# Kernel tuning notes

Hardware: AMD Instinct MI355X
Metric: run time of the kernel (lower is better)

The kernel has to match this reference:

```python
import jax, jax.numpy as jnp
import numpy as np

N_NODES = 100000
N_EDGES = 1600000
D_IN = 128
D_OUT = 128


def setup_inputs() -> dict:
    key = jax.random.key(0)
    k1, k2, k3 = jax.random.split(key, 3)
    x = jax.random.normal(k1, (N_NODES, D_IN), dtype=jnp.float32)
    edge_index = jax.random.randint(k2, (2, N_EDGES), 0, N_NODES, dtype=jnp.int64)
    # Xavier-uniform-like init for weight (matches nn.init.xavier_uniform_ scale)
    limit = float(np.sqrt(6.0 / (D_IN + D_OUT)))
    weight = jax.random.uniform(k3, (D_IN, D_OUT), dtype=jnp.float32,
                                minval=-limit, maxval=limit)
    bias = jnp.zeros((D_OUT,), dtype=jnp.float32)
    return {"x": x, "edge_index": edge_index, "weight": weight, "bias": bias}


def reference(x, edge_index, weight, bias):
    num_nodes = x.shape[0]
    src = edge_index[0]  # edge_index_i: gather side
    dst = edge_index[1]  # edge_index_j: scatter side

    # Degree of each node counted over src endpoints.
    deg = jax.ops.segment_sum(jnp.ones_like(src, dtype=x.dtype), src,
                              num_segments=num_nodes)
    # deg^{-1/2} with inf -> 0 for isolated nodes.
    deg_safe = jnp.where(deg > 0, deg, jnp.ones_like(deg))
    deg_inv_sqrt = jnp.where(deg > 0, jax.lax.rsqrt(deg_safe), jnp.zeros_like(deg))

    norm = deg_inv_sqrt[src] * deg_inv_sqrt[dst]  # [E]

    h = x @ weight  # [N, D_OUT]
    # Edge-parallel gather, scale, scatter-add.
    msgs = norm[:, None] * h[src]  # [E, D_OUT]
    out = jax.ops.segment_sum(msgs, dst, num_segments=num_nodes)  # [N, D_OUT]
    return out + bias
```

## Files before the change

### kernel.cpp

```cpp
#include <hip/hip_runtime.h>

#define D 128
#define CAP 64
#define STRIP_LOG 15
#define STRIP (1 << STRIP_LOG)
#define WORDS_LOG (STRIP_LOG - 2)
#define WORDS (1 << WORDS_LOG)
#define NCHUNK 128
#define LDK 132

typedef __attribute__((ext_vector_type(8))) short bf16x8;
typedef __attribute__((ext_vector_type(4))) float f32x4;

__device__ __forceinline__ unsigned f2bf(float f) {
    unsigned u = __float_as_uint(f);
    return (u + 0x7fffu + ((u >> 16) & 1u)) >> 16;
}

__device__ __forceinline__ int chunk_size(int n_edges) {
    return (((n_edges + NCHUNK - 1) / NCHUNK) + 3) & ~3;
}

__global__ __launch_bounds__(256) void k_histA(const int* __restrict__ src,
                                               const int* __restrict__ dst,
                                               unsigned* __restrict__ pb_s,
                                               unsigned* __restrict__ pb_d, int n_edges) {
    int strip = blockIdx.x / NCHUNK, chunk = blockIdx.x % NCHUNK;
    int lo = strip << STRIP_LOG;
    __shared__ unsigned hs[WORDS];
    __shared__ unsigned hd[WORDS];
    for (int i = threadIdx.x; i < WORDS; i += 256) { hs[i] = 0; hd[i] = 0; }
    __syncthreads();

    int csz = chunk_size(n_edges);
    int beg = chunk * csz;
    int end = min(beg + csz, n_edges);
    if (beg < end) {
        int aend = beg + ((end - beg) & ~3);
        for (int i = beg + threadIdx.x * 4; i + 3 < aend; i += 1024) {
            int4 s = *(const int4*)(src + i);
            int4 d = *(const int4*)(dst + i);
            unsigned b;
            b = (unsigned)(s.x - lo); if (b < STRIP) atomicAdd(&hs[b >> 2], 1u << ((b & 3) * 8));
            b = (unsigned)(s.y - lo); if (b < STRIP) atomicAdd(&hs[b >> 2], 1u << ((b & 3) * 8));
            b = (unsigned)(s.z - lo); if (b < STRIP) atomicAdd(&hs[b >> 2], 1u << ((b & 3) * 8));
            b = (unsigned)(s.w - lo); if (b < STRIP) atomicAdd(&hs[b >> 2], 1u << ((b & 3) * 8));
            b = (unsigned)(d.x - lo); if (b < STRIP) atomicAdd(&hd[b >> 2], 1u << ((b & 3) * 8));
            b = (unsigned)(d.y - lo); if (b < STRIP) atomicAdd(&hd[b >> 2], 1u << ((b & 3) * 8));
            b = (unsigned)(d.z - lo); if (b < STRIP) atomicAdd(&hd[b >> 2], 1u << ((b & 3) * 8));
            b = (unsigned)(d.w - lo); if (b < STRIP) atomicAdd(&hd[b >> 2], 1u << ((b & 3) * 8));
        }
        for (int e = aend + threadIdx.x; e < end; e += 256) {
            unsigned bs = (unsigned)(src[e] - lo);
            if (bs < STRIP) atomicAdd(&hs[bs >> 2], 1u << ((bs & 3) * 8));
            unsigned bd = (unsigned)(dst[e] - lo);
            if (bd < STRIP) atomicAdd(&hd[bd >> 2], 1u << ((bd & 3) * 8));
        }
    }
    __syncthreads();
    unsigned* ps = pb_s + (size_t)blockIdx.x * WORDS;
    unsigned* pd = pb_d + (size_t)blockIdx.x * WORDS;
    for (int i = threadIdx.x; i < WORDS; i += 256) { ps[i] = hs[i]; pd[i] = hd[i]; }
}

__global__ __launch_bounds__(256) void k_base_dis(unsigned* __restrict__ pb_d,
                                                  const unsigned* __restrict__ pb_s,
                                                  int* __restrict__ deg_dst,
                                                  float* __restrict__ dis,
                                                  int n, int nwords) {
    int gw = blockIdx.x * 256 + threadIdx.x;
    if (gw >= nwords) return;
    int strip = gw >> WORDS_LOG, widx = gw & (WORDS - 1);
    size_t base = (size_t)strip * NCHUNK * WORDS + widx;

    unsigned run[4] = {0, 0, 0, 0};
    for (int c = 0; c < NCHUNK; ++c) {
        size_t idx = base + (size_t)c * WORDS;
        unsigned v = pb_d[idx];
        pb_d[idx] = run[0] | (run[1] << 8) | (run[2] << 16) | (run[3] << 24);
        run[0] += v & 0xffu;
        run[1] += (v >> 8) & 0xffu;
        run[2] += (v >> 16) & 0xffu;
        run[3] += (v >> 24) & 0xffu;
    }
    int g0 = (strip << STRIP_LOG) + widx * 4;
    if (g0 >= n) return;

    unsigned ss[4] = {0, 0, 0, 0};
    for (int c = 0; c < NCHUNK; ++c) {
        unsigned v = pb_s[base + (size_t)c * WORDS];
        ss[0] += v & 0xffu;
        ss[1] += (v >> 8) & 0xffu;
        ss[2] += (v >> 16) & 0xffu;
        ss[3] += (v >> 24) & 0xffu;
    }
    if (g0 + 3 < n) {
        *(int4*)(deg_dst + g0) = make_int4(run[0], run[1], run[2], run[3]);
        *(float4*)(dis + g0) = make_float4(
            ss[0] ? rsqrtf((float)ss[0]) : 0.0f, ss[1] ? rsqrtf((float)ss[1]) : 0.0f,
            ss[2] ? rsqrtf((float)ss[2]) : 0.0f, ss[3] ? rsqrtf((float)ss[3]) : 0.0f);
    } else {
        #pragma unroll
        for (int j = 0; j < 4; ++j)
            if (g0 + j < n) {
                deg_dst[g0 + j] = run[j];
                dis[g0 + j] = ss[j] ? rsqrtf((float)ss[j]) : 0.0f;
            }
    }
}

__global__ __launch_bounds__(256) void k_placeB(const int* __restrict__ src,
                                                const int* __restrict__ dst,
                                                const unsigned* __restrict__ pb_d,
                                                int* __restrict__ epad, int n_edges) {
    int strip = blockIdx.x / NCHUNK, chunk = blockIdx.x % NCHUNK;
    int lo = strip << STRIP_LOG;
    __shared__ unsigned cur[WORDS];
    const unsigned* cb = pb_d + (size_t)blockIdx.x * WORDS;
    for (int i = threadIdx.x; i < WORDS; i += 256) cur[i] = cb[i];
    __syncthreads();

    int csz = chunk_size(n_edges);
    int beg = chunk * csz;
    int end = min(beg + csz, n_edges);
    if (beg < end) {
        int aend = beg + ((end - beg) & ~3);
        for (int i = beg + threadIdx.x * 4; i + 3 < aend; i += 1024) {
            int4 s = *(const int4*)(src + i);
            int4 d = *(const int4*)(dst + i);
            unsigned b, o, r;
            b = (unsigned)(d.x - lo);
            if (b < STRIP) {
                o = atomicAdd(&cur[b >> 2], 1u << ((b & 3) * 8));
                r = (o >> ((b & 3) * 8)) & 0xffu;
                if (r < CAP) epad[(((unsigned)lo + b) << 6) + r] = s.x;
            }
            b = (unsigned)(d.y - lo);
            if (b < STRIP) {
                o = atomicAdd(&cur[b >> 2], 1u << ((b & 3) * 8));
                r = (o >> ((b & 3) * 8)) & 0xffu;
                if (r < CAP) epad[(((unsigned)lo + b) << 6) + r] = s.y;
            }
            b = (unsigned)(d.z - lo);
            if (b < STRIP) {
                o = atomicAdd(&cur[b >> 2], 1u << ((b & 3) * 8));
                r = (o >> ((b & 3) * 8)) & 0xffu;
                if (r < CAP) epad[(((unsigned)lo + b) << 6) + r] = s.z;
            }
            b = (unsigned)(d.w - lo);
            if (b < STRIP) {
                o = atomicAdd(&cur[b >> 2], 1u << ((b & 3) * 8));
                r = (o >> ((b & 3) * 8)) & 0xffu;
                if (r < CAP) epad[(((unsigned)lo + b) << 6) + r] = s.w;
            }
        }
        for (int e = aend + threadIdx.x; e < end; e += 256) {
            unsigned b = (unsigned)(dst[e] - lo);
            if (b < STRIP) {
                unsigned o = atomicAdd(&cur[b >> 2], 1u << ((b & 3) * 8));
                unsigned r = (o >> ((b & 3) * 8)) & 0xffu;
                if (r < CAP) epad[(((unsigned)lo + b) << 6) + r] = src[e];
            }
        }
    }
}

__global__ __launch_bounds__(256) void k_gemm(const float* __restrict__ x,
                                              const float* __restrict__ w,
                                              const float* __restrict__ dis,
                                              unsigned* __restrict__ hb, int nrows) {
    __shared__ __align__(16) unsigned short smem[2][128][LDK];
    int tid = threadIdx.x;
    int row0 = blockIdx.x * 128;
    int nr = min(128, nrows - row0);

    {
        const float4* w4 = (const float4*)w;
        for (int i = tid; i < 128 * 32; i += 256) {
            int k = i >> 5, n0 = (i & 31) * 4;
            float4 v = w4[i];
            smem[1][n0 + 0][k] = (unsigned short)f2bf(v.x);
            smem[1][n0 + 1][k] = (unsigned short)f2bf(v.y);
            smem[1][n0 + 2][k] = (unsigned short)f2bf(v.z);
            smem[1][n0 + 3][k] = (unsigned short)f2bf(v.w);
        }
    }
    {
        const float4* x4 = (const float4*)(x + (size_t)row0 * D);
        for (int i = tid; i < 128 * 32; i += 256) {
            int r = i >> 5, c4 = (i & 31) * 4;
            float4 v = (r < nr) ? x4[i] : make_float4(0.f, 0.f, 0.f, 0.f);
            unsigned lo = f2bf(v.x) | (f2bf(v.y) << 16);
            unsigned hi = f2bf(v.z) | (f2bf(v.w) << 16);
            *(uint2*)&smem[0][r][c4] = make_uint2(lo, hi);
        }
    }
    __syncthreads();

    int lane = tid & 63, wv = tid >> 6;
    int m = lane & 15, quad = lane >> 4;
    int rbase = wv * 32;

    f32x4 acc[2][8] = {};
    #pragma unroll
    for (int kt = 0; kt < 4; ++kt) {
        int k0 = kt * 32 + quad * 8;
        bf16x8 a0 = *(const bf16x8*)&smem[0][rbase + m][k0];
        bf16x8 a1 = *(const bf16x8*)&smem[0][rbase + 16 + m][k0];
        bf16x8 b[8];
        #pragma unroll
        for (int ct = 0; ct < 8; ++ct)
            b[ct] = *(const bf16x8*)&smem[1][ct * 16 + m][k0];
        #pragma unroll
        for (int ct = 0; ct < 8; ++ct) {
            acc[0][ct] = __builtin_amdgcn_mfma_f32_16x16x32_bf16(a0, b[ct], acc[0][ct], 0, 0, 0);
            acc[1][ct] = __builtin_amdgcn_mfma_f32_16x16x32_bf16(a1, b[ct], acc[1][ct], 0, 0, 0);
        }
    }

    __syncthreads();
    float* sO = (float*)smem;
    #pragma unroll
    for (int rt = 0; rt < 2; ++rt)
        #pragma unroll
        for (int ct = 0; ct < 8; ++ct)
            #pragma unroll
            for (int reg = 0; reg < 4; ++reg)
                sO[(rbase + rt * 16 + quad * 4 + reg) * LDK + ct * 16 + m] = acc[rt][ct][reg];
    __syncthreads();

    int r = tid >> 1, hf = tid & 1;
    if (r < nr) {
        float dn = dis[row0 + r];
        const float* so = sO + r * LDK + hf * 64;
        unsigned* hrow = hb + (size_t)(row0 + r) * 64 + hf * 32;
        #pragma unroll
        for (int j = 0; j < 8; ++j) {
            float2 p0 = *(const float2*)(so + j * 8 + 0);
            float2 p1 = *(const float2*)(so + j * 8 + 2);
            float2 p2 = *(const float2*)(so + j * 8 + 4);
            float2 p3 = *(const float2*)(so + j * 8 + 6);
            uint4 o;
            o.x = f2bf(dn * p0.x) | (f2bf(dn * p0.y) << 16);
            o.y = f2bf(dn * p1.x) | (f2bf(dn * p1.y) << 16);
            o.z = f2bf(dn * p2.x) | (f2bf(dn * p2.y) << 16);
            o.w = f2bf(dn * p3.x) | (f2bf(dn * p3.y) << 16);
            *(uint4*)(hrow + j * 4) = o;
        }
    }
}

#define ACC8(u) do { \
    ax[0] += __uint_as_float((u).x << 16); ax[1] += __uint_as_float((u).x & 0xffff0000u); \
    ax[2] += __uint_as_float((u).y << 16); ax[3] += __uint_as_float((u).y & 0xffff0000u); \
    ax[4] += __uint_as_float((u).z << 16); ax[5] += __uint_as_float((u).z & 0xffff0000u); \
    ax[6] += __uint_as_float((u).w << 16); ax[7] += __uint_as_float((u).w & 0xffff0000u); } while (0)

__global__ __launch_bounds__(256) void k_accum(const int* __restrict__ epad,
                                               const int* __restrict__ degd,
                                               const uint4* __restrict__ hb4,
                                               const float* __restrict__ dis,
                                               const float* __restrict__ bias,
                                               float* __restrict__ out, int n) {
    int wid = threadIdx.x >> 6, lane = threadIdx.x & 63;
    int node = blockIdx.x * 4 + wid;
    if (node >= n) return;
    int deg = min(degd[node], CAP);
    int g = lane >> 4, c = lane & 15;
    const int* ep = epad + (size_t)node * CAP;

    float ax[8] = {0.f, 0.f, 0.f, 0.f, 0.f, 0.f, 0.f, 0.f};
    int e = g;
    for (; e + 12 < deg; e += 16) {
        int s0 = ep[e];
        int s1 = ep[e + 4];
        int s2 = ep[e + 8];
        int s3 = ep[e + 12];
        uint4 u0 = hb4[(size_t)s0 * 16 + c];
        uint4 u1 = hb4[(size_t)s1 * 16 + c];
        uint4 u2 = hb4[(size_t)s2 * 16 + c];
        uint4 u3 = hb4[(size_t)s3 * 16 + c];
        ACC8(u0); ACC8(u1); ACC8(u2); ACC8(u3);
    }
    for (; e < deg; e += 4) {
        int s0 = ep[e];
        uint4 u0 = hb4[(size_t)s0 * 16 + c];
        ACC8(u0);
    }

    #pragma unroll
    for (int k = 0; k < 8; ++k) {
        ax[k] += __shfl_xor(ax[k], 16, 64);
        ax[k] += __shfl_xor(ax[k], 32, 64);
    }

    if (g == 0) {
        float dn = dis[node];
        float4 b0 = ((const float4*)bias)[c * 2];
        float4 b1 = ((const float4*)bias)[c * 2 + 1];
        float4 o0 = make_float4(fmaf(dn, ax[0], b0.x), fmaf(dn, ax[1], b0.y),
                                fmaf(dn, ax[2], b0.z), fmaf(dn, ax[3], b0.w));
        float4 o1 = make_float4(fmaf(dn, ax[4], b1.x), fmaf(dn, ax[5], b1.y),
                                fmaf(dn, ax[6], b1.z), fmaf(dn, ax[7], b1.w));
        float4* op = (float4*)(out + (size_t)node * D) + c * 2;
        op[0] = o0;
        op[1] = o1;
    }
}

extern "C" void kernel_launch(void* const* d_in, const int* in_sizes, int n_in,
                              void* d_out, int out_size, void* d_ws, size_t ws_size,
                              hipStream_t stream) {
    const float* x    = (const float*)d_in[0];
    const int*   ei   = (const int*)d_in[1];
    const float* w    = (const float*)d_in[2];
    const float* bias = (const float*)d_in[3];
    float* out = (float*)d_out;

    int n_edges = in_sizes[1] / 2;
    int n_nodes = in_sizes[0] / D;
    const int* src = ei;
    const int* dst = ei + n_edges;

    int nstrips = (n_nodes + STRIP - 1) >> STRIP_LOG;
    int nwords = nstrips * WORDS;

    char* ws = (char*)d_ws;
    unsigned* hb = (unsigned*)ws;      ws += (size_t)n_nodes * 64 * sizeof(unsigned);
    int* epad    = (int*)ws;           ws += (size_t)n_nodes * CAP * sizeof(int);
    int* deg_dst = (int*)ws;           ws += (size_t)n_nodes * sizeof(int);
    float* dis   = (float*)ws;         ws += (size_t)n_nodes * sizeof(float);
    unsigned* pb_s = (unsigned*)ws;    ws += (size_t)nstrips * NCHUNK * WORDS * sizeof(unsigned);
    unsigned* pb_d = (unsigned*)ws;

    k_histA<<<nstrips * NCHUNK, 256, 0, stream>>>(src, dst, pb_s, pb_d, n_edges);
    k_base_dis<<<(nwords + 255) / 256, 256, 0, stream>>>(pb_d, pb_s, deg_dst, dis,
                                                         n_nodes, nwords);
    k_gemm<<<(n_nodes + 127) / 128, 256, 0, stream>>>(x, w, dis, hb, n_nodes);
    k_placeB<<<nstrips * NCHUNK, 256, 0, stream>>>(src, dst, pb_d, epad, n_edges);
    k_accum<<<(n_nodes + 3) / 4, 256, 0, stream>>>(epad, deg_dst, (const uint4*)hb,
                                                   dis, bias, out, n_nodes);
}
```

Measured before the change: 261.1 us.

## Load GEMM A operand directly from global and use per-wave output staging

The GEMM kernel no longer stages the x tile through shared memory. Each lane loads its fp32 A fragments straight from global memory and converts them to bf16 in registers. The shared output buffer is now a private 16-row slice per wave, which removes the block-wide barriers after the MFMA loop, and the weight padding changes to 136. This cuts LDS traffic and synchronisation, and the smaller LDS footprint may allow more blocks per CU. In exchange, the global x loads are less coalesced, and the per-wave staging depends on wave-local ordering through a waitcnt rather than a barrier.

New measurement: 252.1 us. -3.5%, faster.

```diff
diff --git a/kernel.cpp b/kernel.cpp
--- a/kernel.cpp
+++ b/kernel.cpp
@@ -7,7 +7,8 @@
 #define WORDS_LOG (STRIP_LOG - 2)
 #define WORDS (1 << WORDS_LOG)
 #define NCHUNK 128
-#define LDK 132
+#define LDW 136
+#define LDO 132
 
 typedef __attribute__((ext_vector_type(8))) short bf16x8;
 typedef __attribute__((ext_vector_type(4))) float f32x4;
@@ -169,48 +170,54 @@
                                               const float* __restrict__ w,
                                               const float* __restrict__ dis,
                                               unsigned* __restrict__ hb, int nrows) {
-    __shared__ __align__(16) unsigned short smem[2][128][LDK];
+    __shared__ __align__(16) unsigned short wt[128][LDW];
+    __shared__ __align__(16) float sOut[4][16][LDO];
     int tid = threadIdx.x;
-    int row0 = blockIdx.x * 128;
-    int nr = min(128, nrows - row0);
 
     {
         const float4* w4 = (const float4*)w;
-        for (int i = tid; i < 128 * 32; i += 256) {
+        #pragma unroll
+        for (int it = 0; it < 16; ++it) {
+            int i = tid + it * 256;
             int k = i >> 5, n0 = (i & 31) * 4;
             float4 v = w4[i];
-            smem[1][n0 + 0][k] = (unsigned short)f2bf(v.x);
-            smem[1][n0 + 1][k] = (unsigned short)f2bf(v.y);
-            smem[1][n0 + 2][k] = (unsigned short)f2bf(v.z);
-            smem[1][n0 + 3][k] = (unsigned short)f2bf(v.w);
-        }
-    }
-    {
-        const float4* x4 = (const float4*)(x + (size_t)row0 * D);
-        for (int i = tid; i < 128 * 32; i += 256) {
-            int r = i >> 5, c4 = (i & 31) * 4;
-            float4 v = (r < nr) ? x4[i] : make_float4(0.f, 0.f, 0.f, 0.f);
-            unsigned lo = f2bf(v.x) | (f2bf(v.y) << 16);
-            unsigned hi = f2bf(v.z) | (f2bf(v.w) << 16);
-            *(uint2*)&smem[0][r][c4] = make_uint2(lo, hi);
+            wt[n0 + 0][k] = (unsigned short)f2bf(v.x);
+            wt[n0 + 1][k] = (unsigned short)f2bf(v.y);
+            wt[n0 + 2][k] = (unsigned short)f2bf(v.z);
+            wt[n0 + 3][k] = (unsigned short)f2bf(v.w);
         }
     }
     __syncthreads();
 
     int lane = tid & 63, wv = tid >> 6;
     int m = lane & 15, quad = lane >> 4;
-    int rbase = wv * 32;
+    int rbase = blockIdx.x * 128 + wv * 32;
+
+    int r0 = rbase + m, r1 = rbase + 16 + m;
+    const float* pa0 = x + (size_t)(r0 < nrows ? r0 : 0) * D;
+    const float* pa1 = x + (size_t)(r1 < nrows ? r1 : 0) * D;
 
     f32x4 acc[2][8] = {};
     #pragma unroll
     for (int kt = 0; kt < 4; ++kt) {
         int k0 = kt * 32 + quad * 8;
-        bf16x8 a0 = *(const bf16x8*)&smem[0][rbase + m][k0];
-        bf16x8 a1 = *(const bf16x8*)&smem[0][rbase + 16 + m][k0];
+        float4 a0l = *(const float4*)(pa0 + k0);
+        float4 a0h = *(const float4*)(pa0 + k0 + 4);
+        float4 a1l = *(const float4*)(pa1 + k0);
+        float4 a1h = *(const float4*)(pa1 + k0 + 4);
+        bf16x8 a0, a1;
+        a0[0] = (short)f2bf(a0l.x); a0[1] = (short)f2bf(a0l.y);
+        a0[2] = (short)f2bf(a0l.z); a0[3] = (short)f2bf(a0l.w);
+        a0[4] = (short)f2bf(a0h.x); a0[5] = (short)f2bf(a0h.y);
+        a0[6] = (short)f2bf(a0h.z); a0[7] = (short)f2bf(a0h.w);
+        a1[0] = (short)f2bf(a1l.x); a1[1] = (short)f2bf(a1l.y);
+        a1[2] = (short)f2bf(a1l.z); a1[3] = (short)f2bf(a1l.w);
+        a1[4] = (short)f2bf(a1h.x); a1[5] = (short)f2bf(a1h.y);
+        a1[6] = (short)f2bf(a1h.z); a1[7] = (short)f2bf(a1h.w);
         bf16x8 b[8];
         #pragma unroll
         for (int ct = 0; ct < 8; ++ct)
-            b[ct] = *(const bf16x8*)&smem[1][ct * 16 + m][k0];
+            b[ct] = *(const bf16x8*)&wt[ct * 16 + m][k0];
         #pragma unroll
         for (int ct = 0; ct < 8; ++ct) {
             acc[0][ct] = __builtin_amdgcn_mfma_f32_16x16x32_bf16(a0, b[ct], acc[0][ct], 0, 0, 0);
@@ -218,35 +225,35 @@
         }
     }
 
-    __syncthreads();
-    float* sO = (float*)smem;
+    float* so = &sOut[wv][0][0];
+    int ri = lane >> 2, qc = lane & 3;
     #pragma unroll
-    for (int rt = 0; rt < 2; ++rt)
+    for (int rt = 0; rt < 2; ++rt) {
         #pragma unroll
         for (int ct = 0; ct < 8; ++ct)
             #pragma unroll
             for (int reg = 0; reg < 4; ++reg)
-                sO[(rbase + rt * 16 + quad * 4 + reg) * LDK + ct * 16 + m] = acc[rt][ct][reg];
-    __syncthreads();
-
-    int r = tid >> 1, hf = tid & 1;
-    if (r < nr) {
-        float dn = dis[row0 + r];
-        const float* so = sO + r * LDK + hf * 64;
-        unsigned* hrow = hb + (size_t)(row0 + r) * 64 + hf * 32;
-        #pragma unroll
-        for (int j = 0; j < 8; ++j) {
-            float2 p0 = *(const float2*)(so + j * 8 + 0);
-            float2 p1 = *(const float2*)(so + j * 8 + 2);
-            float2 p2 = *(const float2*)(so + j * 8 + 4);
-            float2 p3 = *(const float2*)(so + j * 8 + 6);
-            uint4 o;
-            o.x = f2bf(dn * p0.x) | (f2bf(dn * p0.y) << 16);
-            o.y = f2bf(dn * p1.x) | (f2bf(dn * p1.y) << 16);
-            o.z = f2bf(dn * p2.x) | (f2bf(dn * p2.y) << 16);
-            o.w = f2bf(dn * p3.x) | (f2bf(dn * p3.y) << 16);
-            *(uint4*)(hrow + j * 4) = o;
-        }
+                so[(quad * 4 + reg) * LDO + ct * 16 + m] = acc[rt][ct][reg];
+        int row = rbase + rt * 16 + ri;
+        if (row < nrows) {
+            float dn = dis[row];
+            const float* sr = so + ri * LDO + qc * 32;
+            unsigned* hrow = hb + (size_t)row * 64 + qc * 16;
+            #pragma unroll
+            for (int j = 0; j < 4; ++j) {
+                float2 p0 = *(const float2*)(sr + j * 8 + 0);
+                float2 p1 = *(const float2*)(sr + j * 8 + 2);
+                float2 p2 = *(const float2*)(sr + j * 8 + 4);
+                float2 p3 = *(const float2*)(sr + j * 8 + 6);
+                uint4 o;
+                o.x = f2bf(dn * p0.x) | (f2bf(dn * p0.y) << 16);
+                o.y = f2bf(dn * p1.x) | (f2bf(dn * p1.y) << 16);
+                o.z = f2bf(dn * p2.x) | (f2bf(dn * p2.y) << 16);
+                o.w = f2bf(dn * p3.x) | (f2bf(dn * p3.y) << 16);
+                *(uint4*)(hrow + j * 4) = o;
+            }
+        }
+        __builtin_amdgcn_s_waitcnt(0);
     }
 }
 
```
